# Kernel optimization log

Measured on AMD Instinct MI355X. Metric: run time of the kernel, lower is better.

The kernel has to match this reference:

```python
import jax, jax.numpy as jnp
import numpy as np

B, S, D, H = 2, 2048, 1024, 16
HD = D // H  # 64


def setup_inputs() -> dict:
    key = jax.random.key(0)
    ks = jax.random.split(key, 7)
    s = 1.0 / np.sqrt(HD)
    return {
        "x": jax.random.normal(ks[0], (B, S, D), dtype=jnp.float32),
        "Wq": jax.random.normal(ks[1], (H, HD, HD), dtype=jnp.float32) * s,
        "bq": jax.random.normal(ks[2], (H, HD), dtype=jnp.float32) * 0.01,
        "Wk": jax.random.normal(ks[3], (H, HD, HD), dtype=jnp.float32) * s,
        "bk": jax.random.normal(ks[4], (H, HD), dtype=jnp.float32) * 0.01,
        "Wv": jax.random.normal(ks[5], (H, HD, HD), dtype=jnp.float32) * s,
        "bv": jax.random.normal(ks[6], (H, HD), dtype=jnp.float32) * 0.01,
    }


def reference(x, Wq, bq, Wk, bk, Wv, bv):
    b, s, d = x.shape
    h, hd, _ = Wq.shape
    # Faithful to torch: x.view(B, H, S, hd) is a raw reshape (mixes seq positions
    # across heads), NOT a transpose-based head split.
    xh = x.reshape(b, h, s, hd)
    # torch Linear: y @ W.T + b, with W of shape (out, in)
    q = jnp.einsum('bhse,hde->bhsd', xh, Wq) + bq[None, :, None, :]
    k = jnp.einsum('bhse,hde->bhsd', xh, Wk) + bk[None, :, None, :]
    v = jnp.einsum('bhse,hde->bhsd', xh, Wv) + bv[None, :, None, :]
    scale = 1.0 / jnp.sqrt(jnp.asarray(d / h, dtype=jnp.float32))
    attn = jax.nn.softmax(jnp.einsum('bhqd,bhkd->bhqk', q, k) * scale, axis=-1)
    out = jnp.einsum('bhqk,bhkd->bhqd', attn, v)
    # torch.cat over heads along last dim == transpose then merge
    return out.transpose(0, 2, 1, 3).reshape(b, s, d)
```

## Files before the change

kernel.cpp:

```cpp
#include <hip/hip_runtime.h>
#include <hip/hip_bf16.h>

#define BATCH 2
#define SEQ   2048
#define DMODEL 1024
#define NH    16
#define HD    64
#define QSCALE 0.1803368801111602f

typedef __attribute__((ext_vector_type(8))) short bf16x8;
typedef __attribute__((ext_vector_type(4))) float f32x4;

__device__ __forceinline__ ushort f2bf(float f) {
    union { float f; unsigned u; } v; v.f = f;
    return (ushort)((v.u + 0x8000u) >> 16);
}

__device__ __forceinline__ unsigned pack2bf_t(float a, float b) {
    union { float f; unsigned u; } x, y; x.f = a; y.f = b;
    return __builtin_amdgcn_perm(y.u, x.u, 0x07060302u);
}

__device__ __forceinline__ float exp2r(float x) {
#if __has_builtin(__builtin_amdgcn_exp2f)
    return __builtin_amdgcn_exp2f(x);
#else
    return exp2f(x);
#endif
}

#define MFMA(a, b, c) __builtin_amdgcn_mfma_f32_16x16x32_bf16((a), (b), (c), 0, 0, 0)

__global__ __launch_bounds__(256) void qkv_kernel(
    const float* __restrict__ x,
    const float* __restrict__ Wq, const float* __restrict__ bq,
    const float* __restrict__ Wk, const float* __restrict__ bk,
    const float* __restrict__ Wv, const float* __restrict__ bv,
    ushort* __restrict__ Qo, ushort* __restrict__ Kf, ushort* __restrict__ Vf)
{
    const int bid = blockIdx.x;
    const int ch  = bid & 15;
    const int bh  = bid >> 4;
    const int h   = bh & (NH - 1);

    __shared__ ushort Xs[64 * 72];
    __shared__ ushort Ws[3 * 64 * 72];

    const int tid  = threadIdx.x;
    const int wave = tid >> 6, lane = tid & 63;
    const int ln16 = lane & 15, quad = lane >> 4;

    const float* wsrc[3] = { Wq + h * 4096, Wk + h * 4096, Wv + h * 4096 };
    for (int m = 0; m < 3; ++m)
        for (int i = 0; i < 4; ++i) {
            int idx = tid + 256 * i;
            float4 v = ((const float4*)wsrc[m])[idx];
            if (m == 0) { v.x *= QSCALE; v.y *= QSCALE; v.z *= QSCALE; v.w *= QSCALE; }
            int row = idx >> 4, c4 = (idx & 15) * 4;
            ushort4 o;
            o.x = f2bf(v.x); o.y = f2bf(v.y); o.z = f2bf(v.z); o.w = f2bf(v.w);
            *(ushort4*)&Ws[m * 64 * 72 + row * 72 + c4] = o;
        }

    const float* bias[3] = { bq + h * 64, bk + h * 64, bv + h * 64 };
    ushort* Eb = Xs;

    for (int tt = 0; tt < 2; ++tt) {
        const int st = ch * 2 + tt;
        __syncthreads();

        const float* xp = x + (size_t)bh * (SEQ * HD) + (size_t)st * 64 * HD;
        for (int i = 0; i < 4; ++i) {
            int idx = tid + 256 * i;
            float4 v = ((const float4*)xp)[idx];
            int row = idx >> 4, c4 = (idx & 15) * 4;
            ushort4 o;
            o.x = f2bf(v.x); o.y = f2bf(v.y); o.z = f2bf(v.z); o.w = f2bf(v.w);
            *(ushort4*)&Xs[row * 72 + c4] = o;
        }
        __syncthreads();

        bf16x8 afr[2];
        for (int ks = 0; ks < 2; ++ks)
            afr[ks] = *(const bf16x8*)&Xs[(wave * 16 + ln16) * 72 + ks * 32 + quad * 8];
        __syncthreads();

        for (int m = 0; m < 3; ++m) {
            f32x4 acc[4];
            for (int nt = 0; nt < 4; ++nt) {
                acc[nt] = (f32x4){0.f, 0.f, 0.f, 0.f};
                for (int ks = 0; ks < 2; ++ks) {
                    bf16x8 bfr = *(const bf16x8*)&Ws[m * 64 * 72 + (nt * 16 + ln16) * 72 + ks * 32 + quad * 8];
                    acc[nt] = MFMA(afr[ks], bfr, acc[nt]);
                }
            }
            if (m < 2) {
                for (int nt = 0; nt < 4; ++nt) {
                    float bb = bias[m][nt * 16 + ln16];
                    if (m == 0) bb *= QSCALE;
                    for (int r = 0; r < 4; ++r)
                        Eb[(wave * 16 + quad * 4 + r) * 72 + nt * 16 + ln16] = f2bf(acc[nt][r] + bb);
                }
                __syncthreads();
                if (m == 0) {
                    ushort* dst = Qo + (size_t)bh * SEQ * HD + (size_t)st * 64 * HD;
                    for (int i = 0; i < 2; ++i) {
                        int idx = tid + 256 * i;
                        int row = idx >> 3, c8 = (idx & 7) * 8;
                        *(bf16x8*)&dst[row * 64 + c8] = *(const bf16x8*)&Eb[row * 72 + c8];
                    }
                } else {
                    ushort* dst = Kf + ((size_t)bh * 32 + st) * 4096;
                    for (int i = 0; i < 2; ++i) {
                        int idx8 = tid + 256 * i;
                        int l2 = idx8 & 63, chunk = idx8 >> 6;
                        int nt = chunk >> 1, ks = chunk & 1;
                        int qd = l2 >> 4, l16 = l2 & 15;
                        *(bf16x8*)&dst[(size_t)idx8 * 8] =
                            *(const bf16x8*)&Eb[(nt * 16 + l16) * 72 + ks * 32 + qd * 8];
                    }
                }
                __syncthreads();
            } else {
                for (int nt = 0; nt < 4; ++nt) {
                    float bb = bias[2][nt * 16 + ln16];
                    ushort4 o;
                    o.x = f2bf(acc[nt][0] + bb);
                    o.y = f2bf(acc[nt][1] + bb);
                    o.z = f2bf(acc[nt][2] + bb);
                    o.w = f2bf(acc[nt][3] + bb);
                    *(ushort4*)&Eb[(nt * 16 + ln16) * 72 + wave * 16 + quad * 4] = o;
                }
                __syncthreads();
                ushort* dst = Vf + ((size_t)bh * 32 + st) * 4096;
                for (int i = 0; i < 2; ++i) {
                    int idx8 = tid + 256 * i;
                    int l2 = idx8 & 63, chunk = idx8 >> 6;
                    int nt = chunk >> 1, ks = chunk & 1;
                    int qd = l2 >> 4, l16 = l2 & 15;
                    *(bf16x8*)&dst[(size_t)idx8 * 8] =
                        *(const bf16x8*)&Eb[(nt * 16 + l16) * 72 + ks * 32 + qd * 8];
                }
            }
        }
    }
}

__global__ __launch_bounds__(128, 2) void attn_kernel(
    const ushort* __restrict__ Q, const ushort* __restrict__ Kf,
    const ushort* __restrict__ Vf, float* __restrict__ out)
{
    const int bid = blockIdx.x;
    const int qt  = bid & 31;
    const int bh  = bid >> 5;
    const int h   = bh & (NH - 1), b = bh >> 4;

    __shared__ ushort Ps[2][2][32 * 72];

    const int tid = threadIdx.x, wave = tid >> 6, lane = tid & 63;
    const int ln16 = lane & 15, quad = lane >> 4;

    bf16x8 qfr[2][2];
#pragma unroll
    for (int g = 0; g < 2; ++g) {
        const ushort* Qg = Q + ((size_t)bh * SEQ + qt * 64 + wave * 32 + g * 16 + ln16) * HD;
        qfr[g][0] = *(const bf16x8*)&Qg[quad * 8];
        qfr[g][1] = *(const bf16x8*)&Qg[32 + quad * 8];
    }

    const bf16x8* kfp = (const bf16x8*)(Kf + (size_t)bh * 32 * 4096) + lane;
    const bf16x8* vfp = (const bf16x8*)(Vf + (size_t)bh * 32 * 4096) + lane;

    bf16x8 ones;
#pragma unroll
    for (int j = 0; j < 8; ++j) ones[j] = (short)0x3F80;

    f32x4 accO[2][4], accL[2];
#pragma unroll
    for (int g = 0; g < 2; ++g) {
        accL[g] = (f32x4){0.f, 0.f, 0.f, 0.f};
#pragma unroll
        for (int nt = 0; nt < 4; ++nt) accO[g][nt] = (f32x4){0.f, 0.f, 0.f, 0.f};
    }

    bf16x8 kf[8], vf[8];
#pragma unroll
    for (int c = 0; c < 8; ++c) kf[c] = kfp[c * 64];
    kfp += 512;

    for (int kt = 0; kt < 32; ++kt) {
        const int cur = kt & 1;

        bf16x8 pf[2][2];
        if (kt > 0) {
            const ushort* Pr = Ps[wave][1 - cur];
#pragma unroll
            for (int g = 0; g < 2; ++g) {
                pf[g][0] = *(const bf16x8*)&Pr[(g * 16 + ln16) * 72 + quad * 8];
                pf[g][1] = *(const bf16x8*)&Pr[(g * 16 + ln16) * 72 + 32 + quad * 8];
            }
        }

        f32x4 sacc[2][4];
#pragma unroll
        for (int nt = 0; nt < 4; ++nt)
#pragma unroll
            for (int g = 0; g < 2; ++g) {
                f32x4 a = {0.f, 0.f, 0.f, 0.f};
                a = MFMA(kf[nt * 2],     qfr[g][0], a);
                a = MFMA(kf[nt * 2 + 1], qfr[g][1], a);
                sacc[g][nt] = a;
            }

        if (kt < 31) {
#pragma unroll
            for (int c = 0; c < 8; ++c) kf[c] = kfp[c * 64];
            kfp += 512;
        }

        if (kt > 0) {
#pragma unroll
            for (int nt = 0; nt < 4; ++nt)
#pragma unroll
                for (int g = 0; g < 2; ++g) {
                    accO[g][nt] = MFMA(vf[nt * 2],     pf[g][0], accO[g][nt]);
                    accO[g][nt] = MFMA(vf[nt * 2 + 1], pf[g][1], accO[g][nt]);
                }
#pragma unroll
            for (int g = 0; g < 2; ++g) {
                accL[g] = MFMA(ones, pf[g][0], accL[g]);
                accL[g] = MFMA(ones, pf[g][1], accL[g]);
            }
        }

#pragma unroll
        for (int c = 0; c < 8; ++c) vf[c] = vfp[c * 64];
        vfp += 512;

        ushort* Pw = Ps[wave][cur];
#pragma unroll
        for (int g = 0; g < 2; ++g)
#pragma unroll
            for (int nt = 0; nt < 4; ++nt) {
                float p0 = exp2r(sacc[g][nt][0]);
                float p1 = exp2r(sacc[g][nt][1]);
                float p2 = exp2r(sacc[g][nt][2]);
                float p3 = exp2r(sacc[g][nt][3]);
                uint2 pk;
                pk.x = pack2bf_t(p0, p1);
                pk.y = pack2bf_t(p2, p3);
                *(uint2*)&Pw[(g * 16 + ln16) * 72 + nt * 16 + quad * 4] = pk;
            }
    }

    {
        const ushort* Pr = Ps[wave][1];
        bf16x8 pf[2][2];
#pragma unroll
        for (int g = 0; g < 2; ++g) {
            pf[g][0] = *(const bf16x8*)&Pr[(g * 16 + ln16) * 72 + quad * 8];
            pf[g][1] = *(const bf16x8*)&Pr[(g * 16 + ln16) * 72 + 32 + quad * 8];
        }
#pragma unroll
        for (int nt = 0; nt < 4; ++nt)
#pragma unroll
            for (int g = 0; g < 2; ++g) {
                accO[g][nt] = MFMA(vf[nt * 2],     pf[g][0], accO[g][nt]);
                accO[g][nt] = MFMA(vf[nt * 2 + 1], pf[g][1], accO[g][nt]);
            }
#pragma unroll
        for (int g = 0; g < 2; ++g) {
            accL[g] = MFMA(ones, pf[g][0], accL[g]);
            accL[g] = MFMA(ones, pf[g][1], accL[g]);
        }
    }

#pragma unroll
    for (int g = 0; g < 2; ++g) {
        float rinv = 1.0f / accL[g][0];
        float* ob = out + ((size_t)b * SEQ + qt * 64 + wave * 32 + g * 16 + ln16) * DMODEL + h * HD;
#pragma unroll
        for (int nt = 0; nt < 4; ++nt) {
            float4 o;
            o.x = accO[g][nt][0] * rinv;
            o.y = accO[g][nt][1] * rinv;
            o.z = accO[g][nt][2] * rinv;
            o.w = accO[g][nt][3] * rinv;
            *(float4*)&ob[nt * 16 + quad * 4] = o;
        }
    }
}

extern "C" void kernel_launch(void* const* d_in, const int* in_sizes, int n_in,
                              void* d_out, int out_size, void* d_ws, size_t ws_size,
                              hipStream_t stream) {
    const float* x  = (const float*)d_in[0];
    const float* Wq = (const float*)d_in[1];
    const float* bq = (const float*)d_in[2];
    const float* Wk = (const float*)d_in[3];
    const float* bk = (const float*)d_in[4];
    const float* Wv = (const float*)d_in[5];
    const float* bv = (const float*)d_in[6];

    const size_t nElem = (size_t)BATCH * NH * SEQ * HD;
    ushort* Qw = (ushort*)d_ws;
    ushort* Kw = Qw + nElem;
    ushort* Vw = Kw + nElem;

    qkv_kernel<<<32 * 16, 256, 0, stream>>>(
        x, Wq, bq, Wk, bk, Wv, bv, Qw, Kw, Vw);
    attn_kernel<<<BATCH * NH * (SEQ / 64), 128, 0, stream>>>(
        Qw, Kw, Vw, (float*)d_out);
}
```

Before: 129.6 us.

## Split attention work across four waves and compute row sums with VALU

The attention kernel now uses 256 threads (four waves), each handling 16 query rows instead of 32. Per-wave registers and MFMA count drop, which should allow higher occupancy. The ones-vector MFMA used for the softmax denominator is replaced by a per-lane float sum of the unrounded exp values plus a cross-lane shuffle reduction. The trade-off is that each K/V fragment is now loaded from global memory by four waves instead of two, doubling K/V traffic per block, and the denominator no longer uses the same bf16-rounded P that feeds the PV product.

```diff
diff --git a/kernel.cpp b/kernel.cpp
--- a/kernel.cpp
+++ b/kernel.cpp
@@ -146,7 +146,7 @@
     }
 }
 
-__global__ __launch_bounds__(128, 2) void attn_kernel(
+__global__ __launch_bounds__(256, 4) void attn_kernel(
     const ushort* __restrict__ Q, const ushort* __restrict__ Kf,
     const ushort* __restrict__ Vf, float* __restrict__ out)
 {
@@ -155,33 +155,23 @@
     const int bh  = bid >> 5;
     const int h   = bh & (NH - 1), b = bh >> 4;
 
-    __shared__ ushort Ps[2][2][32 * 72];
+    __shared__ ushort Ps[4][2][16 * 72];
 
     const int tid = threadIdx.x, wave = tid >> 6, lane = tid & 63;
     const int ln16 = lane & 15, quad = lane >> 4;
 
-    bf16x8 qfr[2][2];
-#pragma unroll
-    for (int g = 0; g < 2; ++g) {
-        const ushort* Qg = Q + ((size_t)bh * SEQ + qt * 64 + wave * 32 + g * 16 + ln16) * HD;
-        qfr[g][0] = *(const bf16x8*)&Qg[quad * 8];
-        qfr[g][1] = *(const bf16x8*)&Qg[32 + quad * 8];
-    }
+    const ushort* Qg = Q + ((size_t)bh * SEQ + qt * 64 + wave * 16 + ln16) * HD;
+    bf16x8 qfr[2];
+    qfr[0] = *(const bf16x8*)&Qg[quad * 8];
+    qfr[1] = *(const bf16x8*)&Qg[32 + quad * 8];
 
     const bf16x8* kfp = (const bf16x8*)(Kf + (size_t)bh * 32 * 4096) + lane;
     const bf16x8* vfp = (const bf16x8*)(Vf + (size_t)bh * 32 * 4096) + lane;
 
-    bf16x8 ones;
-#pragma unroll
-    for (int j = 0; j < 8; ++j) ones[j] = (short)0x3F80;
-
-    f32x4 accO[2][4], accL[2];
-#pragma unroll
-    for (int g = 0; g < 2; ++g) {
-        accL[g] = (f32x4){0.f, 0.f, 0.f, 0.f};
-#pragma unroll
-        for (int nt = 0; nt < 4; ++nt) accO[g][nt] = (f32x4){0.f, 0.f, 0.f, 0.f};
-    }
+    float lsum = 0.f;
+    f32x4 accO[4];
+#pragma unroll
+    for (int nt = 0; nt < 4; ++nt) accO[nt] = (f32x4){0.f, 0.f, 0.f, 0.f};
 
     bf16x8 kf[8], vf[8];
 #pragma unroll
@@ -191,26 +181,21 @@
     for (int kt = 0; kt < 32; ++kt) {
         const int cur = kt & 1;
 
-        bf16x8 pf[2][2];
+        bf16x8 pf[2];
         if (kt > 0) {
             const ushort* Pr = Ps[wave][1 - cur];
-#pragma unroll
-            for (int g = 0; g < 2; ++g) {
-                pf[g][0] = *(const bf16x8*)&Pr[(g * 16 + ln16) * 72 + quad * 8];
-                pf[g][1] = *(const bf16x8*)&Pr[(g * 16 + ln16) * 72 + 32 + quad * 8];
-            }
-        }
-
-        f32x4 sacc[2][4];
-#pragma unroll
-        for (int nt = 0; nt < 4; ++nt)
-#pragma unroll
-            for (int g = 0; g < 2; ++g) {
-                f32x4 a = {0.f, 0.f, 0.f, 0.f};
-                a = MFMA(kf[nt * 2],     qfr[g][0], a);
-                a = MFMA(kf[nt * 2 + 1], qfr[g][1], a);
-                sacc[g][nt] = a;
-            }
+            pf[0] = *(const bf16x8*)&Pr[ln16 * 72 + quad * 8];
+            pf[1] = *(const bf16x8*)&Pr[ln16 * 72 + 32 + quad * 8];
+        }
+
+        f32x4 sacc[4];
+#pragma unroll
+        for (int nt = 0; nt < 4; ++nt) {
+            f32x4 a = {0.f, 0.f, 0.f, 0.f};
+            a = MFMA(kf[nt * 2],     qfr[0], a);
+            a = MFMA(kf[nt * 2 + 1], qfr[1], a);
+            sacc[nt] = a;
+        }
 
         if (kt < 31) {
 #pragma unroll
@@ -220,16 +205,9 @@
 
         if (kt > 0) {
 #pragma unroll
-            for (int nt = 0; nt < 4; ++nt)
-#pragma unroll
-                for (int g = 0; g < 2; ++g) {
-                    accO[g][nt] = MFMA(vf[nt * 2],     pf[g][0], accO[g][nt]);
-                    accO[g][nt] = MFMA(vf[nt * 2 + 1], pf[g][1], accO[g][nt]);
-                }
-#pragma unroll
-            for (int g = 0; g < 2; ++g) {
-                accL[g] = MFMA(ones, pf[g][0], accL[g]);
-                accL[g] = MFMA(ones, pf[g][1], accL[g]);
+            for (int nt = 0; nt < 4; ++nt) {
+                accO[nt] = MFMA(vf[nt * 2],     pf[0], accO[nt]);
+                accO[nt] = MFMA(vf[nt * 2 + 1], pf[1], accO[nt]);
             }
         }
 
@@ -238,56 +216,46 @@
         vfp += 512;
 
         ushort* Pw = Ps[wave][cur];
-#pragma unroll
-        for (int g = 0; g < 2; ++g)
-#pragma unroll
-            for (int nt = 0; nt < 4; ++nt) {
-                float p0 = exp2r(sacc[g][nt][0]);
-                float p1 = exp2r(sacc[g][nt][1]);
-                float p2 = exp2r(sacc[g][nt][2]);
-                float p3 = exp2r(sacc[g][nt][3]);
-                uint2 pk;
-                pk.x = pack2bf_t(p0, p1);
-                pk.y = pack2bf_t(p2, p3);
-                *(uint2*)&Pw[(g * 16 + ln16) * 72 + nt * 16 + quad * 4] = pk;
-            }
+        float rs = 0.f;
+#pragma unroll
+        for (int nt = 0; nt < 4; ++nt) {
+            float p0 = exp2r(sacc[nt][0]);
+            float p1 = exp2r(sacc[nt][1]);
+            float p2 = exp2r(sacc[nt][2]);
+            float p3 = exp2r(sacc[nt][3]);
+            rs += (p0 + p1) + (p2 + p3);
+            uint2 pk;
+            pk.x = pack2bf_t(p0, p1);
+            pk.y = pack2bf_t(p2, p3);
+            *(uint2*)&Pw[ln16 * 72 + nt * 16 + quad * 4] = pk;
+        }
+        lsum += rs;
     }
 
     {
         const ushort* Pr = Ps[wave][1];
-        bf16x8 pf[2][2];
-#pragma unroll
-        for (int g = 0; g < 2; ++g) {
-            pf[g][0] = *(const bf16x8*)&Pr[(g * 16 + ln16) * 72 + quad * 8];
-            pf[g][1] = *(const bf16x8*)&Pr[(g * 16 + ln16) * 72 + 32 + quad * 8];
-        }
-#pragma unroll
-        for (int nt = 0; nt < 4; ++nt)
-#pragma unroll
-            for (int g = 0; g < 2; ++g) {
-                accO[g][nt] = MFMA(vf[nt * 2],     pf[g][0], accO[g][nt]);
-                accO[g][nt] = MFMA(vf[nt * 2 + 1], pf[g][1], accO[g][nt]);
-            }
-#pragma unroll
-        for (int g = 0; g < 2; ++g) {
-            accL[g] = MFMA(ones, pf[g][0], accL[g]);
-            accL[g] = MFMA(ones, pf[g][1], accL[g]);
-        }
-    }
-
-#pragma unroll
-    for (int g = 0; g < 2; ++g) {
-        float rinv = 1.0f / accL[g][0];
-        float* ob = out + ((size_t)b * SEQ + qt * 64 + wave * 32 + g * 16 + ln16) * DMODEL + h * HD;
+        bf16x8 pf[2];
+        pf[0] = *(const bf16x8*)&Pr[ln16 * 72 + quad * 8];
+        pf[1] = *(const bf16x8*)&Pr[ln16 * 72 + 32 + quad * 8];
 #pragma unroll
         for (int nt = 0; nt < 4; ++nt) {
-            float4 o;
-            o.x = accO[g][nt][0] * rinv;
-            o.y = accO[g][nt][1] * rinv;
-            o.z = accO[g][nt][2] * rinv;
-            o.w = accO[g][nt][3] * rinv;
-            *(float4*)&ob[nt * 16 + quad * 4] = o;
-        }
+            accO[nt] = MFMA(vf[nt * 2],     pf[0], accO[nt]);
+            accO[nt] = MFMA(vf[nt * 2 + 1], pf[1], accO[nt]);
+        }
+    }
+
+    lsum += __shfl_xor(lsum, 16, 64);
+    lsum += __shfl_xor(lsum, 32, 64);
+    float rinv = 1.0f / lsum;
+    float* ob = out + ((size_t)b * SEQ + qt * 64 + wave * 16 + ln16) * DMODEL + h * HD;
+#pragma unroll
+    for (int nt = 0; nt < 4; ++nt) {
+        float4 o;
+        o.x = accO[nt][0] * rinv;
+        o.y = accO[nt][1] * rinv;
+        o.z = accO[nt][2] * rinv;
+        o.w = accO[nt][3] * rinv;
+        *(float4*)&ob[nt * 16 + quad * 4] = o;
     }
 }
 
@@ -309,6 +277,6 @@
 
     qkv_kernel<<<32 * 16, 256, 0, stream>>>(
         x, Wq, bq, Wk, bk, Wv, bv, Qw, Kw, Vw);
-    attn_kernel<<<BATCH * NH * (SEQ / 64), 128, 0, stream>>>(
+    attn_kernel<<<BATCH * NH * (SEQ / 64), 256, 0, stream>>>(
         Qw, Kw, Vw, (float*)d_out);
 }
```

New measurement: 150.4 us. +16.0%, slower.
